# Performance work log

Hardware: AMD Instinct MI355X
Metric: run time of the kernel (lower is better)

The kernel has to match this reference:

```python
import jax, jax.numpy as jnp
import numpy as np

N_NODES = 50000
N_EDGES = 800000
IN_F = 64
OUT_F = 64


def setup_inputs() -> dict:
    key = jax.random.key(0)
    k_x, k_r, k_c, k_v, k_w, k_b = jax.random.split(key, 6)
    x = jax.random.normal(k_x, (N_NODES, IN_F), dtype=jnp.float32)
    edge_row = jax.random.randint(k_r, (N_EDGES,), 0, N_NODES, dtype=jnp.int32)
    edge_col = jax.random.randint(k_c, (N_EDGES,), 0, N_NODES, dtype=jnp.int32)
    edge_val = jax.random.uniform(k_v, (N_EDGES,), dtype=jnp.float32)
    weight = jax.random.normal(k_w, (IN_F, OUT_F), dtype=jnp.float32) * (2.0 / (IN_F + OUT_F)) ** 0.5
    bias = jax.random.normal(k_b, (OUT_F,), dtype=jnp.float32) * 0.1
    return {"x": x, "edge_row": edge_row, "edge_col": edge_col,
            "edge_val": edge_val, "weight": weight, "bias": bias}


def reference(x, edge_row, edge_col, edge_val, weight, bias):
    # support = x @ W  : dense GEMM  [N, out]
    support = jnp.matmul(x, weight)
    # output = spmm(adj, support): for each edge (r, c, v): out[r] += v * support[c]
    gathered = support[edge_col] * edge_val[:, None]  # [E, out]
    output = jax.ops.segment_sum(gathered, edge_row, num_segments=N_NODES)
    return output + bias
```

## Files before the change

kernel.cpp:

```cpp
#include <hip/hip_runtime.h>
#include <hip/hip_bf16.h>
#include <hip/hip_cooperative_groups.h>

namespace cg = cooperative_groups;

#define N_NODES 50000
#define N_EDGES 800000
#define NF 64
#define BUCK_SHIFT 6
#define BUCK_SIZE 64
#define NBUK 782
#define CAP 1280
#define CHUNK 4096
#define BIN_BLOCKS 196
#define GRID 1024
#define GEMM_BLOCKS (GRID - BIN_BLOCKS)
#define EPT (CHUNK / 256)
#define PER ((NBUK + 255) / 256)

#define SMEM_BYTES (CHUNK * 8 + NBUK * 4 * 2 + 32)

__device__ __forceinline__ void phase1(
    const float* __restrict__ x, const int* __restrict__ erow,
    const int* __restrict__ ecol, const float* __restrict__ eval,
    const float* __restrict__ w, int2* __restrict__ stage,
    int* __restrict__ gcur, __hip_bfloat16* __restrict__ support,
    char* smemraw) {
  const int tid = threadIdx.x;
  const int lane = tid & 63;
  const int wave = tid >> 6;

  if (blockIdx.x < BIN_BLOCKS) {
    int2* sorted = (int2*)smemraw;
    int* hist = (int*)(smemraw + CHUNK * 8);
    int* offs = hist + NBUK;
    int* wsum = offs + NBUK;

    for (int t = tid; t < NBUK; t += 256) hist[t] = 0;
    __syncthreads();

    const int e0 = blockIdx.x * CHUNK;
    const int e1 = min(e0 + CHUNK, N_EDGES);

    int rj[EPT], cj[EPT];
    float vj[EPT];
#pragma unroll
    for (int j = 0; j < EPT; ++j) {
      const int e = e0 + tid + j * 256;
      const bool ok = e < e1;
      rj[j] = ok ? erow[e] : -1;
      cj[j] = ok ? ecol[e] : 0;
      vj[j] = ok ? eval[e] : 0.f;
      if (ok) atomicAdd(&hist[rj[j] >> BUCK_SHIFT], 1);
    }
    __syncthreads();

    int loc[PER];
    int tsum = 0;
    const int i0 = tid * PER;
#pragma unroll
    for (int j = 0; j < PER; ++j) {
      const int idx = i0 + j;
      const int v = (idx < NBUK) ? hist[idx] : 0;
      loc[j] = tsum;
      tsum += v;
    }
    int sc = tsum;
#pragma unroll
    for (int off = 1; off < 64; off <<= 1) {
      const int up = __shfl_up(sc, off, 64);
      if (lane >= off) sc += up;
    }
    if (lane == 63) wsum[wave] = sc;
    __syncthreads();
    int woff = 0;
#pragma unroll
    for (int k = 0; k < 4; ++k) woff += (k < wave) ? wsum[k] : 0;
    const int texcl = woff + sc - tsum;

#pragma unroll
    for (int j = 0; j < PER; ++j) {
      const int idx = i0 + j;
      if (idx < NBUK) {
        const int o = texcl + loc[j];
        hist[idx] = o;
        offs[idx] = o;
      }
    }
    __syncthreads();

#pragma unroll
    for (int j = 0; j < EPT; ++j) {
      if (rj[j] >= 0) {
        const int b = rj[j] >> BUCK_SHIFT;
        const int p = atomicAdd(&hist[b], 1);
        sorted[p] = make_int2(
            (int)(((unsigned)rj[j] << 16) | (unsigned)cj[j]),
            __float_as_int(vj[j]));
      }
    }
    __syncthreads();

    for (int idx = tid; idx < NBUK; idx += 256) {
      const int c = hist[idx] - offs[idx];
      int delta = 0;
      if (c > 0) delta = atomicAdd(&gcur[idx], c) - offs[idx];
      hist[idx] = delta;
    }
    __syncthreads();

    const int n = e1 - e0;
    for (int i = tid; i < n; i += 256) {
      const int2 m = sorted[i];
      const unsigned b = ((unsigned)m.x) >> (16 + BUCK_SHIFT);
      const int s = i + hist[b];
      if (s < CAP) stage[(size_t)b * CAP + s] = m;
    }
  } else {
    float wcol[NF];
#pragma unroll
    for (int k = 0; k < NF; ++k) wcol[k] = w[k * NF + lane];

    const int wid = (blockIdx.x - BIN_BLOCKS) * 4 + wave;
    const int nw = GEMM_BLOCKS * 4;
    for (int row = wid; row < N_NODES; row += 2 * nw) {
      const int rA = __builtin_amdgcn_readfirstlane(row);
      const int rB_raw = row + nw;
      const bool hasB = rB_raw < N_NODES;
      const int rB = __builtin_amdgcn_readfirstlane(hasB ? rB_raw : rA);
      const float* xA = x + (size_t)rA * NF;
      const float* xB = x + (size_t)rB * NF;
      float a0 = 0.f, a1 = 0.f, a2 = 0.f, a3 = 0.f;
      float b0 = 0.f, b1 = 0.f, b2 = 0.f, b3 = 0.f;
#pragma unroll
      for (int k = 0; k < NF; k += 4) {
        a0 = fmaf(xA[k + 0], wcol[k + 0], a0);
        b0 = fmaf(xB[k + 0], wcol[k + 0], b0);
        a1 = fmaf(xA[k + 1], wcol[k + 1], a1);
        b1 = fmaf(xB[k + 1], wcol[k + 1], b1);
        a2 = fmaf(xA[k + 2], wcol[k + 2], a2);
        b2 = fmaf(xB[k + 2], wcol[k + 2], b2);
        a3 = fmaf(xA[k + 3], wcol[k + 3], a3);
        b3 = fmaf(xB[k + 3], wcol[k + 3], b3);
      }
      support[(size_t)rA * NF + lane] = __float2bfloat16((a0 + a1) + (a2 + a3));
      if (hasB)
        support[(size_t)rB * NF + lane] =
            __float2bfloat16((b0 + b1) + (b2 + b3));
    }
  }
}

__device__ __forceinline__ void phase2(
    const __hip_bfloat16* __restrict__ support, const int2* __restrict__ stage,
    const int* __restrict__ gcur, const float* __restrict__ bias,
    float* __restrict__ out, char* smemraw) {
  const int b = blockIdx.x;
  if (b >= NBUK) return;
  int2* srt = (int2*)smemraw;
  int* rcnt = (int*)(smemraw + CAP * 8);
  int* rofs = rcnt + BUCK_SIZE;
  int* rcur = rofs + BUCK_SIZE;
  const int tid = threadIdx.x;
  const int lane = tid & 63;
  const int wave = tid >> 6;

  if (tid < BUCK_SIZE) rcnt[tid] = 0;
  __syncthreads();

  const int cnt = min(gcur[b], CAP);

  int2 mreg[5];
#pragma unroll
  for (int q = 0; q < 5; ++q) {
    const int i = tid + q * 256;
    if (i < cnt) {
      const int2 m = stage[(size_t)b * CAP + i];
      mreg[q] = m;
      atomicAdd(&rcnt[(((unsigned)m.x) >> 16) & (BUCK_SIZE - 1)], 1);
    }
  }
  __syncthreads();

  if (tid < 64) {
    const int v = rcnt[lane];
    int s2 = v;
#pragma unroll
    for (int off = 1; off < 64; off <<= 1) {
      const int up = __shfl_up(s2, off, 64);
      if (lane >= off) s2 += up;
    }
    rofs[lane] = s2 - v;
    rcur[lane] = s2 - v;
  }
  __syncthreads();

#pragma unroll
  for (int q = 0; q < 5; ++q) {
    if (tid + q * 256 < cnt) {
      const int p =
          atomicAdd(&rcur[(((unsigned)mreg[q].x) >> 16) & (BUCK_SIZE - 1)], 1);
      srt[p] = mreg[q];
    }
  }
  __syncthreads();

  const int grp = lane >> 4;
  const int sub = lane & 15;
  const int row0 = b << BUCK_SHIFT;
  const float4 bv4 = reinterpret_cast<const float4*>(bias)[sub];
#pragma unroll 2
  for (int rr = 0; rr < 16; ++rr) {
    const int rl = wave * 16 + rr;
    const int row = row0 + rl;
    if (row >= N_NODES) break;
    const int s = __builtin_amdgcn_readfirstlane(rofs[rl]);
    const int e = __builtin_amdgcn_readfirstlane(rofs[rl] + rcnt[rl]);
    float a0 = 0.f, a1 = 0.f, a2 = 0.f, a3 = 0.f;
    int i = s;
    for (; i + 16 <= e; i += 16) {
#pragma unroll
      for (int q = 0; q < 4; ++q) {
        const int2 m = srt[i + 4 * q + grp];
        const float v = __int_as_float(m.y);
        const uint2 t = *reinterpret_cast<const uint2*>(
            support + (size_t)(m.x & 0xFFFF) * NF + sub * 4);
        a0 = fmaf(v, __int_as_float(t.x << 16), a0);
        a1 = fmaf(v, __int_as_float((int)(t.x & 0xFFFF0000u)), a1);
        a2 = fmaf(v, __int_as_float(t.y << 16), a2);
        a3 = fmaf(v, __int_as_float((int)(t.y & 0xFFFF0000u)), a3);
      }
    }
    for (; i < e; i += 4) {
      const int idx = i + grp;
      if (idx < e) {
        const int2 m = srt[idx];
        const float v = __int_as_float(m.y);
        const uint2 t = *reinterpret_cast<const uint2*>(
            support + (size_t)(m.x & 0xFFFF) * NF + sub * 4);
        a0 = fmaf(v, __int_as_float(t.x << 16), a0);
        a1 = fmaf(v, __int_as_float((int)(t.x & 0xFFFF0000u)), a1);
        a2 = fmaf(v, __int_as_float(t.y << 16), a2);
        a3 = fmaf(v, __int_as_float((int)(t.y & 0xFFFF0000u)), a3);
      }
    }
    a0 += __shfl_xor(a0, 16, 64);
    a1 += __shfl_xor(a1, 16, 64);
    a2 += __shfl_xor(a2, 16, 64);
    a3 += __shfl_xor(a3, 16, 64);
    a0 += __shfl_xor(a0, 32, 64);
    a1 += __shfl_xor(a1, 32, 64);
    a2 += __shfl_xor(a2, 32, 64);
    a3 += __shfl_xor(a3, 32, 64);
    if (grp == 0) {
      float4 o;
      o.x = a0 + bv4.x;
      o.y = a1 + bv4.y;
      o.z = a2 + bv4.z;
      o.w = a3 + bv4.w;
      reinterpret_cast<float4*>(out + (size_t)row * NF)[sub] = o;
    }
  }
}

__global__ __launch_bounds__(256, 4) void fused(
    const float* __restrict__ x, const int* __restrict__ erow,
    const int* __restrict__ ecol, const float* __restrict__ eval,
    const float* __restrict__ w, const float* __restrict__ bias,
    __hip_bfloat16* __restrict__ support, int2* __restrict__ stage,
    int* __restrict__ gcur, float* __restrict__ out) {
  __shared__ __align__(16) char smem[SMEM_BYTES];
  phase1(x, erow, ecol, eval, w, stage, gcur, support, smem);
  __threadfence();
  cg::this_grid().sync();
  phase2(support, stage, gcur, bias, out, smem);
}

__global__ __launch_bounds__(256, 4) void k_phase1(
    const float* __restrict__ x, const int* __restrict__ erow,
    const int* __restrict__ ecol, const float* __restrict__ eval,
    const float* __restrict__ w, int2* __restrict__ stage,
    int* __restrict__ gcur, __hip_bfloat16* __restrict__ support) {
  __shared__ __align__(16) char smem[SMEM_BYTES];
  phase1(x, erow, ecol, eval, w, stage, gcur, support, smem);
}

__global__ __launch_bounds__(256) void k_phase2(
    const __hip_bfloat16* __restrict__ support, const int2* __restrict__ stage,
    const int* __restrict__ gcur, const float* __restrict__ bias,
    float* __restrict__ out) {
  __shared__ __align__(16) char smem[CAP * 8 + BUCK_SIZE * 4 * 3];
  phase2(support, stage, gcur, bias, out, smem);
}

extern "C" void kernel_launch(void* const* d_in, const int* in_sizes, int n_in,
                              void* d_out, int out_size, void* d_ws,
                              size_t ws_size, hipStream_t stream) {
  const float* x = (const float*)d_in[0];
  const int* erow = (const int*)d_in[1];
  const int* ecol = (const int*)d_in[2];
  const float* eval = (const float*)d_in[3];
  const float* w = (const float*)d_in[4];
  const float* bias = (const float*)d_in[5];
  float* out = (float*)d_out;

  char* ws = (char*)d_ws;
  __hip_bfloat16* support = (__hip_bfloat16*)(ws);
  int2* stage = (int2*)(ws + 6400000);
  int* gcur = (int*)(ws + 6400000 + 8007680);

  hipMemsetAsync(gcur, 0, NBUK * sizeof(int), stream);

  static int coop = -1;
  if (coop < 0) {
    int nb = 0;
    hipError_t oe =
        hipOccupancyMaxActiveBlocksPerMultiprocessor(&nb, fused, 256, 0);
    coop = (oe == hipSuccess && nb >= 4) ? 1 : 0;
  }

  bool launched = false;
  if (coop) {
    void* args[] = {(void*)&x,       (void*)&erow,  (void*)&ecol,
                    (void*)&eval,    (void*)&w,     (void*)&bias,
                    (void*)&support, (void*)&stage, (void*)&gcur,
                    (void*)&out};
    hipError_t le = hipLaunchCooperativeKernel((const void*)fused, dim3(GRID),
                                               dim3(256), args, 0, stream);
    if (le == hipSuccess) {
      launched = true;
    } else {
      coop = 0;
    }
  }
  if (!launched) {
    k_phase1<<<GRID, 256, 0, stream>>>(x, erow, ecol, eval, w, stage, gcur,
                                       support);
    k_phase2<<<NBUK, 256, 0, stream>>>(support, stage, gcur, bias, out);
  }
}
```

Before: 124.7 us.

## Replace cooperative grid-sync kernel with two launches and 512-thread phase2

Drops the cooperative fused kernel and its grid-wide barrier, and always runs the binning/GEMM phase and the SpMM phase as two separate launches. The second kernel now uses 512-thread blocks, with 8 rows per wave instead of 16 and 3 staged entries per thread instead of 5. Empty register slots are marked with a sentinel. This removes the grid-sync cost and the occupancy limits the fused kernel imposed, and gives each bucket more waves to hide gather latency. In exchange it adds a kernel-launch boundary between the phases.

```diff
diff --git a/kernel.cpp b/kernel.cpp
--- a/kernel.cpp
+++ b/kernel.cpp
@@ -1,8 +1,5 @@
 #include <hip/hip_runtime.h>
 #include <hip/hip_bf16.h>
-#include <hip/hip_cooperative_groups.h>
-
-namespace cg = cooperative_groups;
 
 #define N_NODES 50000
 #define N_EDGES 800000
@@ -20,19 +17,19 @@
 
 #define SMEM_BYTES (CHUNK * 8 + NBUK * 4 * 2 + 32)
 
-__device__ __forceinline__ void phase1(
+__global__ __launch_bounds__(256, 4) void k_phase1(
     const float* __restrict__ x, const int* __restrict__ erow,
     const int* __restrict__ ecol, const float* __restrict__ eval,
     const float* __restrict__ w, int2* __restrict__ stage,
-    int* __restrict__ gcur, __hip_bfloat16* __restrict__ support,
-    char* smemraw) {
+    int* __restrict__ gcur, __hip_bfloat16* __restrict__ support) {
+  __shared__ __align__(16) char smem[SMEM_BYTES];
   const int tid = threadIdx.x;
   const int lane = tid & 63;
   const int wave = tid >> 6;
 
   if (blockIdx.x < BIN_BLOCKS) {
-    int2* sorted = (int2*)smemraw;
-    int* hist = (int*)(smemraw + CHUNK * 8);
+    int2* sorted = (int2*)smem;
+    int* hist = (int*)(smem + CHUNK * 8);
     int* offs = hist + NBUK;
     int* wsum = offs + NBUK;
 
@@ -151,16 +148,15 @@
   }
 }
 
-__device__ __forceinline__ void phase2(
+__global__ __launch_bounds__(512) void k_phase2(
     const __hip_bfloat16* __restrict__ support, const int2* __restrict__ stage,
     const int* __restrict__ gcur, const float* __restrict__ bias,
-    float* __restrict__ out, char* smemraw) {
+    float* __restrict__ out) {
+  __shared__ int2 srt[CAP];
+  __shared__ int rcnt[BUCK_SIZE];
+  __shared__ int rofs[BUCK_SIZE];
+  __shared__ int rcur[BUCK_SIZE];
   const int b = blockIdx.x;
-  if (b >= NBUK) return;
-  int2* srt = (int2*)smemraw;
-  int* rcnt = (int*)(smemraw + CAP * 8);
-  int* rofs = rcnt + BUCK_SIZE;
-  int* rcur = rofs + BUCK_SIZE;
   const int tid = threadIdx.x;
   const int lane = tid & 63;
   const int wave = tid >> 6;
@@ -170,10 +166,11 @@
 
   const int cnt = min(gcur[b], CAP);
 
-  int2 mreg[5];
-#pragma unroll
-  for (int q = 0; q < 5; ++q) {
-    const int i = tid + q * 256;
+  int2 mreg[3];
+#pragma unroll
+  for (int q = 0; q < 3; ++q) {
+    const int i = tid + q * 512;
+    mreg[q] = make_int2(-1, 0);
     if (i < cnt) {
       const int2 m = stage[(size_t)b * CAP + i];
       mreg[q] = m;
@@ -196,10 +193,10 @@
   __syncthreads();
 
 #pragma unroll
-  for (int q = 0; q < 5; ++q) {
-    if (tid + q * 256 < cnt) {
-      const int p =
-          atomicAdd(&rcur[(((unsigned)mreg[q].x) >> 16) & (BUCK_SIZE - 1)], 1);
+  for (int q = 0; q < 3; ++q) {
+    if (mreg[q].x != -1) {
+      const int p = atomicAdd(
+          &rcur[(((unsigned)mreg[q].x) >> 16) & (BUCK_SIZE - 1)], 1);
       srt[p] = mreg[q];
     }
   }
@@ -209,9 +206,9 @@
   const int sub = lane & 15;
   const int row0 = b << BUCK_SHIFT;
   const float4 bv4 = reinterpret_cast<const float4*>(bias)[sub];
-#pragma unroll 2
-  for (int rr = 0; rr < 16; ++rr) {
-    const int rl = wave * 16 + rr;
+#pragma unroll
+  for (int rr = 0; rr < 8; ++rr) {
+    const int rl = wave * 8 + rr;
     const int row = row0 + rl;
     if (row >= N_NODES) break;
     const int s = __builtin_amdgcn_readfirstlane(rofs[rl]);
@@ -263,36 +260,6 @@
   }
 }
 
-__global__ __launch_bounds__(256, 4) void fused(
-    const float* __restrict__ x, const int* __restrict__ erow,
-    const int* __restrict__ ecol, const float* __restrict__ eval,
-    const float* __restrict__ w, const float* __restrict__ bias,
-    __hip_bfloat16* __restrict__ support, int2* __restrict__ stage,
-    int* __restrict__ gcur, float* __restrict__ out) {
-  __shared__ __align__(16) char smem[SMEM_BYTES];
-  phase1(x, erow, ecol, eval, w, stage, gcur, support, smem);
-  __threadfence();
-  cg::this_grid().sync();
-  phase2(support, stage, gcur, bias, out, smem);
-}
-
-__global__ __launch_bounds__(256, 4) void k_phase1(
-    const float* __restrict__ x, const int* __restrict__ erow,
-    const int* __restrict__ ecol, const float* __restrict__ eval,
-    const float* __restrict__ w, int2* __restrict__ stage,
-    int* __restrict__ gcur, __hip_bfloat16* __restrict__ support) {
-  __shared__ __align__(16) char smem[SMEM_BYTES];
-  phase1(x, erow, ecol, eval, w, stage, gcur, support, smem);
-}
-
-__global__ __launch_bounds__(256) void k_phase2(
-    const __hip_bfloat16* __restrict__ support, const int2* __restrict__ stage,
-    const int* __restrict__ gcur, const float* __restrict__ bias,
-    float* __restrict__ out) {
-  __shared__ __align__(16) char smem[CAP * 8 + BUCK_SIZE * 4 * 3];
-  phase2(support, stage, gcur, bias, out, smem);
-}
-
 extern "C" void kernel_launch(void* const* d_in, const int* in_sizes, int n_in,
                               void* d_out, int out_size, void* d_ws,
                               size_t ws_size, hipStream_t stream) {
@@ -310,32 +277,7 @@
   int* gcur = (int*)(ws + 6400000 + 8007680);
 
   hipMemsetAsync(gcur, 0, NBUK * sizeof(int), stream);
-
-  static int coop = -1;
-  if (coop < 0) {
-    int nb = 0;
-    hipError_t oe =
-        hipOccupancyMaxActiveBlocksPerMultiprocessor(&nb, fused, 256, 0);
-    coop = (oe == hipSuccess && nb >= 4) ? 1 : 0;
-  }
-
-  bool launched = false;
-  if (coop) {
-    void* args[] = {(void*)&x,       (void*)&erow,  (void*)&ecol,
-                    (void*)&eval,    (void*)&w,     (void*)&bias,
-                    (void*)&support, (void*)&stage, (void*)&gcur,
-                    (void*)&out};
-    hipError_t le = hipLaunchCooperativeKernel((const void*)fused, dim3(GRID),
-                                               dim3(256), args, 0, stream);
-    if (le == hipSuccess) {
-      launched = true;
-    } else {
-      coop = 0;
-    }
-  }
-  if (!launched) {
-    k_phase1<<<GRID, 256, 0, stream>>>(x, erow, ecol, eval, w, stage, gcur,
-                                       support);
-    k_phase2<<<NBUK, 256, 0, stream>>>(support, stage, gcur, bias, out);
-  }
+  k_phase1<<<GRID, 256, 0, stream>>>(x, erow, ecol, eval, w, stage, gcur,
+                                     support);
+  k_phase2<<<NBUK, 512, 0, stream>>>(support, stage, gcur, bias, out);
 }
```

New measurement: 118.9 us. 1.05x faster.
